# Optimization experiments

Hardware: AMD Instinct MI355X
Metric: run time of the kernel (lower is better)

## Reference

```python
import jax, jax.numpy as jnp
import numpy as np

BN_EPS = 1e-5

def setup_inputs() -> dict:
    key = jax.random.key(0)
    ks = jax.random.split(key, 4)
    B, C, H, W = 8, 64, 128, 128
    return {
        "x": jax.random.normal(ks[0], (B, C, H, W), jnp.float32),
        "w_reduce": jax.random.normal(ks[1], (C, C), jnp.float32) * 0.05,
        "b_reduce": jnp.zeros((C,), jnp.float32),
        "bn_gamma": jnp.ones((C,), jnp.float32),
        "bn_beta": jnp.zeros((C,), jnp.float32),
        "w_span": jax.random.normal(ks[2], (9, C), jnp.float32) * 0.05,
        "b_span": jnp.zeros((9,), jnp.float32),
        "w_conv2": jax.random.normal(ks[3], (C, C, 3, 3), jnp.float32) * 0.02,
        "b_conv2": jnp.zeros((C,), jnp.float32),
    }


def _involution(x, w_reduce, b_reduce, bn_gamma, bn_beta, w_span, b_span):
    # Involution2d: in_ch == out_ch so initial_mapping is Identity; groups=1, reduce_ratio=1, stride=1.
    B, C, H, W = x.shape
    # unfold 3x3, pad 1 -> patches [B, C, 9, H, W] (torch unfold ordering: C major, then kh, kw)
    xp = jnp.pad(x, ((0, 0), (0, 0), (1, 1), (1, 1)))
    patches = jnp.stack(
        [xp[:, :, i:i + H, j:j + W] for i in range(3) for j in range(3)], axis=2
    )  # [B, C, 9, H, W]
    # kernel generation: 1x1 conv -> BatchNorm2d (batch stats) -> ReLU -> 1x1 conv
    r = jnp.einsum('oc,bchw->bohw', w_reduce, x) + b_reduce[None, :, None, None]
    mu = r.mean(axis=(0, 2, 3), keepdims=True)
    var = r.var(axis=(0, 2, 3), keepdims=True)
    rn = (r - mu) * jax.lax.rsqrt(var + BN_EPS)
    rn = jax.nn.relu(rn * bn_gamma[None, :, None, None] + bn_beta[None, :, None, None])
    kern = jnp.einsum('kc,bchw->bkhw', w_span, rn) + b_span[None, :, None, None]  # [B, 9, H, W]
    # per-pixel dynamic kernel applied to patches, summed over kernel axis
    return jnp.einsum('bkhw,bckhw->bchw', kern, patches)


def reference(x, w_reduce, b_reduce, bn_gamma, bn_beta, w_span, b_span, w_conv2, b_conv2):
    z = jax.nn.softplus(_involution(x, w_reduce, b_reduce, bn_gamma, bn_beta, w_span, b_span))
    y = jax.lax.conv_general_dilated(z, w_conv2, window_strides=(1, 1), padding=((1, 1), (1, 1)))
    y = y + b_conv2[None, :, None, None]
    return jax.nn.softplus(y)
```

## Files before the change

kernel.cpp:

```cpp
#include <hip/hip_runtime.h>
#include <math.h>

#define H_ 128
#define W_ 128
#define C_ 64
#define B_ 8
#define HW 16384
#define NPIX (B_*HW)

typedef __attribute__((ext_vector_type(8))) short short8;
typedef __attribute__((ext_vector_type(4))) float f32x4;

__device__ __forceinline__ float softplus_fast(float v) {
    return fmaxf(v, 0.f) + __logf(1.f + __expf(-fabsf(v)));
}

__device__ __forceinline__ unsigned short f2bf(float f) {
    unsigned u = __builtin_bit_cast(unsigned, f);
    unsigned r = (u + 0x7fffu + ((u >> 16) & 1u)) >> 16;
    return (unsigned short)r;
}

__device__ __forceinline__ void gl_lds16(const float* g, float* l) {
    __builtin_amdgcn_global_load_lds(
        (const __attribute__((address_space(1))) void*)g,
        (__attribute__((address_space(3))) void*)l, 16, 0, 0);
}

__global__ __launch_bounds__(256) void k0_wtr(const float* __restrict__ w2,
                                              const float* __restrict__ wr,
                                              const float* __restrict__ wspan,
                                              unsigned short* __restrict__ wtr,
                                              unsigned short* __restrict__ wtr1,
                                              unsigned short* __restrict__ wtr2,
                                              float* __restrict__ stats)
{
    int t = blockIdx.x * 256 + threadIdx.x;
    if (t < 256) stats[t] = 0.f;
    if (t < 512) {
        int lane = t & 63, f = t >> 6;
        int mt = f >> 1, kh = f & 1;
        int o  = mt * 16 + (lane & 15);
        int c0 = kh * 32 + ((lane >> 4) << 3);
        uint4 pk;
        unsigned short* pv = (unsigned short*)&pk;
#pragma unroll
        for (int e = 0; e < 8; ++e)
            pv[e] = f2bf(wr[o * C_ + c0 + e]);
        *(uint4*)&wtr1[(size_t)t * 8] = pk;
    } else if (t < 640) {
        int tt = t - 512;
        int lane = tt & 63, kh = tt >> 6;
        int o  = lane & 15;
        int c0 = (kh << 5) + ((lane >> 4) << 3);
        uint4 pk;
        unsigned short* pv = (unsigned short*)&pk;
#pragma unroll
        for (int e = 0; e < 8; ++e)
            pv[e] = (o < 9) ? f2bf(wspan[o * C_ + c0 + e]) : (unsigned short)0;
        *(uint4*)&wtr2[(size_t)tt * 8] = pk;
    }
    if (t >= 4 * 18 * 64) return;
    int lane = t & 63;
    int f    = (t >> 6) % 18;
    int wv   = t / (18 * 64);
    int koff = f >> 1, ch = f & 1;
    int o = wv * 16 + (lane & 15);
    int cb = ch * 32 + ((lane >> 4) << 3);
    uint4 pk;
    unsigned short* pv = (unsigned short*)&pk;
#pragma unroll
    for (int e = 0; e < 8; ++e)
        pv[e] = f2bf(w2[(size_t)o * 576 + (size_t)(cb + e) * 9 + koff]);
    *(uint4*)&wtr[(size_t)t * 8] = pk;
}

__global__ __launch_bounds__(256) void k1_mfma(
    const float* __restrict__ x, const unsigned short* __restrict__ wtr1,
    const float* __restrict__ br, unsigned short* __restrict__ rb,
    float* __restrict__ stats)
{
    __shared__ unsigned short xb[256 * 64];
    __shared__ float brs[C_];
    __shared__ float ls[128];
    int tid = threadIdx.x;
    int blk = blockIdx.x;
    int pid0 = blk << 8;
    int b    = pid0 >> 14;
    int rem0 = pid0 & (HW - 1);
    const float* xbase = x + (((size_t)b * C_) << 14) + rem0;

    if (tid < C_) brs[tid] = br[tid];
    if (tid < 128) ls[tid] = 0.f;

    int p = tid;
#pragma unroll
    for (int m = 0; m < 8; ++m) {
        float tmp[8];
#pragma unroll
        for (int e = 0; e < 8; ++e)
            tmp[e] = xbase[((size_t)(m * 8 + e) << 14) + p];
        unsigned pk[4];
#pragma unroll
        for (int e = 0; e < 4; ++e)
            pk[e] = (unsigned)f2bf(tmp[2 * e]) | ((unsigned)f2bf(tmp[2 * e + 1]) << 16);
        *(uint4*)&xb[(p << 6) + ((m ^ (p & 7)) << 3)] = *(uint4*)pk;
    }

    int wid = tid >> 6, lane = tid & 63;
    int nl  = lane & 15;
    int kg  = lane >> 4;

    short8 af[8];
    const short8* wp = (const short8*)wtr1;
#pragma unroll
    for (int f = 0; f < 8; ++f) af[f] = wp[f * 64 + lane];

    f32x4 acc[4][4];
#pragma unroll
    for (int mt = 0; mt < 4; ++mt)
#pragma unroll
        for (int nt = 0; nt < 4; ++nt) acc[mt][nt] = (f32x4){0.f, 0.f, 0.f, 0.f};

    __syncthreads();

    int nbase = wid << 6;
#pragma unroll
    for (int nt = 0; nt < 4; ++nt) {
        int pp = nbase + (nt << 4) + nl;
#pragma unroll
        for (int kh = 0; kh < 2; ++kh) {
            int m = kh * 4 + kg;
            short8 bf = *(const short8*)&xb[(pp << 6) + ((m ^ (pp & 7)) << 3)];
#pragma unroll
            for (int mt = 0; mt < 4; ++mt)
                acc[mt][nt] = __builtin_amdgcn_mfma_f32_16x16x32_bf16(
                    af[mt * 2 + kh], bf, acc[mt][nt], 0, 0, 0);
        }
    }

    __syncthreads();

    float s_[16], q_[16];
#pragma unroll
    for (int i = 0; i < 16; ++i) { s_[i] = 0.f; q_[i] = 0.f; }

#pragma unroll
    for (int mt = 0; mt < 4; ++mt) {
        int c = (mt << 4) + (kg << 2);
        float b0 = brs[c], b1 = brs[c + 1], b2v = brs[c + 2], b3 = brs[c + 3];
        int chunk = c >> 3;
#pragma unroll
        for (int nt = 0; nt < 4; ++nt) {
            int pp = nbase + (nt << 4) + nl;
            f32x4 a = acc[mt][nt];
            float v0 = a[0] + b0, v1 = a[1] + b1, v2 = a[2] + b2v, v3 = a[3] + b3;
            s_[mt * 4 + 0] += v0; q_[mt * 4 + 0] += v0 * v0;
            s_[mt * 4 + 1] += v1; q_[mt * 4 + 1] += v1 * v1;
            s_[mt * 4 + 2] += v2; q_[mt * 4 + 2] += v2 * v2;
            s_[mt * 4 + 3] += v3; q_[mt * 4 + 3] += v3 * v3;
            unsigned lo = (unsigned)f2bf(v0) | ((unsigned)f2bf(v1) << 16);
            unsigned hi = (unsigned)f2bf(v2) | ((unsigned)f2bf(v3) << 16);
            unsigned* dst = (unsigned*)&xb[(pp << 6) + ((chunk ^ (pp & 7)) << 3) + ((kg & 1) << 2)];
            dst[0] = lo;
            dst[1] = hi;
        }
    }

#pragma unroll
    for (int i = 0; i < 16; ++i) {
#pragma unroll
        for (int m = 1; m <= 8; m <<= 1) {
            s_[i] += __shfl_xor(s_[i], m, 64);
            q_[i] += __shfl_xor(q_[i], m, 64);
        }
    }
    if (nl == 0) {
#pragma unroll
        for (int i = 0; i < 16; ++i) {
            int c = ((i >> 2) << 4) + (kg << 2) + (i & 3);
            atomicAdd(&ls[c], s_[i]);
            atomicAdd(&ls[64 + c], q_[i]);
        }
    }
    __syncthreads();
    if (tid < 128) atomicAdd(&stats[tid], ls[tid]);

    uint4* rp = (uint4*)(rb + ((size_t)(pid0 + p) << 6));
#pragma unroll
    for (int m = 0; m < 8; ++m)
        rp[m] = *(const uint4*)&xb[(p << 6) + ((m ^ (p & 7)) << 3)];
}

__global__ __launch_bounds__(256) void k3_involution(
    const float* __restrict__ x, const unsigned short* __restrict__ rb,
    const float* __restrict__ stats, const float* __restrict__ gamma,
    const float* __restrict__ beta, const unsigned short* __restrict__ wtr2,
    const float* __restrict__ bspan, unsigned short* __restrict__ zb)
{
    __shared__ float xh0[3456], xh1[3456];
    __shared__ unsigned zs[256 * 32];
    __shared__ float a_s[C_], c_s[C_];

    int tid = threadIdx.x;
    if (tid < C_) {
        float inv_n = 1.f / (float)NPIX;
        float mu  = stats[tid] * inv_n;
        float var = stats[C_ + tid] * inv_n - mu * mu;
        float is  = rsqrtf(var + 1e-5f);
        float a   = gamma[tid] * is;
        a_s[tid] = a;
        c_s[tid] = beta[tid] - mu * a;
    }

    int blk = blockIdx.x;
    int b = blk >> 6, t = blk & 63;
    int h0 = (t >> 3) << 4, w0 = (t & 7) << 4;
    int ty = tid >> 4, tx = tid & 15;
    int pix = ((h0 + ty) << 7) + (w0 + tx);
    int pid = (b << 14) + pix;
    const float* xb_ = x + (((size_t)b * C_) << 14);
    const float* zgz = stats + 128;

    int goff[4];
#pragma unroll
    for (int k = 0; k < 4; ++k) {
        int item = (k << 8) + tid;
        int c    = item / 108;
        int rem  = item - c * 108;
        int row  = rem / 6;
        int ii   = rem - row * 6;
        int gh   = h0 + row - 1;
        int gw0  = w0 - 4 + (ii << 2);
        bool ok = (item < 864) && ((unsigned)gh < 128u) && ((unsigned)gw0 < 128u);
        goff[k] = ok ? ((c << 14) + (gh << 7) + gw0) : -1;
    }

    auto stage = [&](int g, float* buf) {
#pragma unroll
        for (int k = 0; k < 4; ++k) {
            if (k < 3 || tid < 96) {
                int item = (k << 8) + tid;
                const float* src = (goff[k] >= 0) ? (xb_ + (g << 17) + goff[k]) : zgz;
                gl_lds16(src, buf + (item << 2));
            }
        }
    };

    int lane = tid & 63;
    int w_  = tid >> 6;
    int nl  = lane & 15;
    int kg  = lane >> 4;
    short8 af0 = ((const short8*)wtr2)[lane];
    short8 af1 = ((const short8*)wtr2)[64 + lane];

    stage(0, xh0);
    __syncthreads();
    stage(1, xh1);

    float aa[2][8], cc[2][8];
#pragma unroll
    for (int kh = 0; kh < 2; ++kh) {
        int cb = (kh << 5) + (kg << 3);
#pragma unroll
        for (int e = 0; e < 8; ++e) { aa[kh][e] = a_s[cb + e]; cc[kh][e] = c_s[cb + e]; }
    }

    f32x4 acc9[4];
#pragma unroll
    for (int nt = 0; nt < 4; ++nt) acc9[nt] = (f32x4){0.f, 0.f, 0.f, 0.f};

#pragma unroll
    for (int nt = 0; nt < 4; ++nt) {
        int prow = h0 + (w_ << 2) + nt;
        int pid2 = (b << 14) + (prow << 7) + w0 + nl;
#pragma unroll
        for (int kh = 0; kh < 2; ++kh) {
            uint4 rv = *(const uint4*)(rb + ((size_t)pid2 << 6) + (kh << 5) + (kg << 3));
            const unsigned* ru = (const unsigned*)&rv;
            unsigned po[4];
#pragma unroll
            for (int e2 = 0; e2 < 4; ++e2) {
                float lo = __builtin_bit_cast(float, ru[e2] << 16);
                float hi = __builtin_bit_cast(float, ru[e2] & 0xffff0000u);
                float r0 = fmaxf(aa[kh][2 * e2]     * lo + cc[kh][2 * e2],     0.f);
                float r1 = fmaxf(aa[kh][2 * e2 + 1] * hi + cc[kh][2 * e2 + 1], 0.f);
                po[e2] = (unsigned)f2bf(r0) | ((unsigned)f2bf(r1) << 16);
            }
            short8 bfrag = __builtin_bit_cast(short8, *(uint4*)po);
            acc9[nt] = __builtin_amdgcn_mfma_f32_16x16x32_bf16(
                kh ? af1 : af0, bfrag, acc9[nt], 0, 0, 0);
        }
    }

    float* kl = (float*)zs;
#pragma unroll
    for (int nt = 0; nt < 4; ++nt) {
        int px = (w_ << 6) + (nt << 4) + nl;
#pragma unroll
        for (int e = 0; e < 4; ++e) {
            int rr = (kg << 2) + e;
            if (rr < 9) kl[px * 9 + rr] = acc9[nt][e];
        }
    }
    __syncthreads();
    float kern[9];
#pragma unroll
    for (int k = 0; k < 9; ++k) kern[k] = kl[tid * 9 + k] + bspan[k];
    __syncthreads();

#pragma unroll 1
    for (int g = 0; g < 8; ++g) {
        if (g >= 1 && g < 7) stage(g + 1, (g & 1) ? xh0 : xh1);
        const float* xf = (g & 1) ? xh1 : xh0;
        unsigned pk[4];
#pragma unroll
        for (int cp = 0; cp < 4; ++cp) {
            const float* p0 = xf + (cp * 2) * 432 + ty * 24 + tx + 3;
            const float* p1 = p0 + 432;
            float acc0 = 0.f, acc1 = 0.f;
#pragma unroll
            for (int i = 0; i < 3; ++i)
#pragma unroll
                for (int j = 0; j < 3; ++j) {
                    float kv = kern[i * 3 + j];
                    acc0 += kv * p0[i * 24 + j];
                    acc1 += kv * p1[i * 24 + j];
                }
            pk[cp] = (unsigned)f2bf(softplus_fast(acc0))
                   | ((unsigned)f2bf(softplus_fast(acc1)) << 16);
        }
        *(uint4*)&zs[(tid << 5) + ((g ^ (tid & 7)) << 2)] = *(uint4*)pk;
        if (g < 7) __syncthreads();
    }

    uint4* zp = (uint4*)(zb + ((size_t)pid << 6));
#pragma unroll
    for (int k = 0; k < 8; ++k)
        zp[k] = *(const uint4*)&zs[(tid << 5) + ((k ^ (tid & 7)) << 2)];
}

__global__ __launch_bounds__(256) void k4_mfma(
    const unsigned short* __restrict__ zb, const unsigned short* __restrict__ wtr,
    const float* __restrict__ b2, float* __restrict__ out)
{
    __shared__ unsigned short zt[324 * 64];
    int tid = threadIdx.x;
    int blk = blockIdx.x;
    int b = blk >> 6;
    int t = blk & 63;
    int h0 = (t >> 3) << 4;
    int w0 = (t & 7) << 4;

    for (int idx = tid; idx < 324 * 8; idx += 256) {
        int p  = idx >> 3;
        int cg = idx & 7;
        int py = p / 18, px = p - py * 18;
        int gh = h0 + py - 1, gw = w0 + px - 1;
        uint4 v = make_uint4(0u, 0u, 0u, 0u);
        if ((unsigned)gh < 128u && (unsigned)gw < 128u)
            v = *(const uint4*)(zb + (((size_t)((b << 14) + (gh << 7) + gw)) << 6) + (cg << 3));
        *(uint4*)&zt[(p << 6) + ((cg ^ (p & 7)) << 3)] = v;
    }

    int wid  = tid >> 6, lane = tid & 63;
    int nl   = lane & 15;
    int kg   = lane >> 4;

    short8 wf[18];
    const short8* wp = (const short8*)wtr;
#pragma unroll
    for (int f = 0; f < 18; ++f)
        wf[f] = wp[(size_t)(wid * 18 + f) * 64 + lane];

    f32x4 acc[16];
#pragma unroll
    for (int nt = 0; nt < 16; ++nt) acc[nt] = (f32x4){0.f, 0.f, 0.f, 0.f};

    __syncthreads();

#pragma unroll
    for (int y = 0; y < 18; ++y) {
        short8 bf[6];
#pragma unroll
        for (int j = 0; j < 3; ++j)
#pragma unroll
            for (int ch = 0; ch < 2; ++ch) {
                int p  = y * 18 + j + nl;
                int cg = ch * 4 + kg;
                bf[j * 2 + ch] = *(const short8*)&zt[(p << 6) + ((cg ^ (p & 7)) << 3)];
            }
#pragma unroll
        for (int i = 0; i < 3; ++i) {
            int nt = y - i;
            if (nt >= 0 && nt < 16) {
#pragma unroll
                for (int j = 0; j < 3; ++j)
#pragma unroll
                    for (int ch = 0; ch < 2; ++ch)
                        acc[nt] = __builtin_amdgcn_mfma_f32_16x16x32_bf16(
                            wf[(i * 3 + j) * 2 + ch], bf[j * 2 + ch], acc[nt], 0, 0, 0);
            }
        }
    }

    float bias[4];
#pragma unroll
    for (int r = 0; r < 4; ++r) bias[r] = b2[(wid << 4) + (kg << 2) + r];

    size_t ob = ((size_t)b) << 20;
#pragma unroll
    for (int nt = 0; nt < 16; ++nt) {
        int h = h0 + nt;
#pragma unroll
        for (int r = 0; r < 4; ++r) {
            int o = (wid << 4) + (kg << 2) + r;
            float v = acc[nt][r] + bias[r];
            out[ob + ((size_t)o << 14) + (h << 7) + w0 + nl] = softplus_fast(v);
        }
    }
}

extern "C" void kernel_launch(void* const* d_in, const int* in_sizes, int n_in,
                              void* d_out, int out_size, void* d_ws, size_t ws_size,
                              hipStream_t stream)
{
    const float* x   = (const float*)d_in[0];
    const float* wr  = (const float*)d_in[1];
    const float* br  = (const float*)d_in[2];
    const float* gam = (const float*)d_in[3];
    const float* bet = (const float*)d_in[4];
    const float* wsp = (const float*)d_in[5];
    const float* bsp = (const float*)d_in[6];
    const float* w2  = (const float*)d_in[7];
    const float* b2  = (const float*)d_in[8];
    float* out = (float*)d_out;

    unsigned short* zb   = (unsigned short*)d_ws;
    unsigned short* wtr  = zb + (size_t)NPIX * C_;
    unsigned short* wtr1 = wtr + 4608 * 8;
    unsigned short* wtr2 = wtr1 + 512 * 8;
    float* stats = (float*)(wtr2 + 128 * 8);

    unsigned short* rb = (unsigned short*)d_out;

    k0_wtr<<<18, 256, 0, stream>>>(w2, wr, wsp, wtr, wtr1, wtr2, stats);
    k1_mfma<<<NPIX / 256, 256, 0, stream>>>(x, wtr1, br, rb, stats);
    k3_involution<<<NPIX / 256, 256, 0, stream>>>(x, rb, stats, gam, bet, wtr2, bsp, zb);
    k4_mfma<<<NPIX / 256, 256, 0, stream>>>(zb, wtr, b2, out);
}
```

Before: 80.84 us.

## Fuse involution and 3x3 conv kernels with halo recompute in shared memory

Merges the involution kernel and the MFMA 3x3 convolution into one kernel. Each block now computes the involution output for an 18x18 halo tile directly into shared memory, so the bf16 intermediate z no longer round-trips through global memory. The cost is recomputing the halo pixels (324 vs 256 per tile), larger x staging (20 rows), and more registers and shared memory per block, which may lower occupancy. The r buffer moves from the output buffer to the workspace.

```diff
diff --git a/kernel.cpp b/kernel.cpp
--- a/kernel.cpp
+++ b/kernel.cpp
@@ -192,14 +192,15 @@
         rp[m] = *(const uint4*)&xb[(p << 6) + ((m ^ (p & 7)) << 3)];
 }
 
-__global__ __launch_bounds__(256) void k3_involution(
+__global__ __launch_bounds__(256) void k34_fused(
     const float* __restrict__ x, const unsigned short* __restrict__ rb,
     const float* __restrict__ stats, const float* __restrict__ gamma,
     const float* __restrict__ beta, const unsigned short* __restrict__ wtr2,
-    const float* __restrict__ bspan, unsigned short* __restrict__ zb)
+    const float* __restrict__ bspan, const unsigned short* __restrict__ wtr,
+    const float* __restrict__ b2, float* __restrict__ out)
 {
-    __shared__ float xh0[3456], xh1[3456];
-    __shared__ unsigned zs[256 * 32];
+    __shared__ float xh0[8 * 20 * 24], xh1[8 * 20 * 24];
+    __shared__ unsigned short zt[324 * 64];
     __shared__ float a_s[C_], c_s[C_];
 
     int tid = threadIdx.x;
@@ -216,9 +217,6 @@
     int blk = blockIdx.x;
     int b = blk >> 6, t = blk & 63;
     int h0 = (t >> 3) << 4, w0 = (t & 7) << 4;
-    int ty = tid >> 4, tx = tid & 15;
-    int pix = ((h0 + ty) << 7) + (w0 + tx);
-    int pid = (b << 14) + pix;
     const float* xb_ = x + (((size_t)b * C_) << 14);
     const float* zgz = stats + 128;
 
@@ -226,20 +224,20 @@
 #pragma unroll
     for (int k = 0; k < 4; ++k) {
         int item = (k << 8) + tid;
-        int c    = item / 108;
-        int rem  = item - c * 108;
+        int c    = item / 120;
+        int rem  = item - c * 120;
         int row  = rem / 6;
         int ii   = rem - row * 6;
-        int gh   = h0 + row - 1;
-        int gw0  = w0 - 4 + (ii << 2);
-        bool ok = (item < 864) && ((unsigned)gh < 128u) && ((unsigned)gw0 < 128u);
-        goff[k] = ok ? ((c << 14) + (gh << 7) + gw0) : -1;
+        int gh   = h0 + row - 2;
+        int gw   = w0 - 4 + (ii << 2);
+        bool ok = (item < 960) && ((unsigned)gh < 128u) && ((unsigned)gw < 128u);
+        goff[k] = ok ? ((c << 14) + (gh << 7) + gw) : -1;
     }
 
     auto stage = [&](int g, float* buf) {
 #pragma unroll
         for (int k = 0; k < 4; ++k) {
-            if (k < 3 || tid < 96) {
+            if (k < 3 || tid < 192) {
                 int item = (k << 8) + tid;
                 const float* src = (goff[k] >= 0) ? (xb_ + (g << 17) + goff[k]) : zgz;
                 gl_lds16(src, buf + (item << 2));
@@ -266,118 +264,125 @@
         for (int e = 0; e < 8; ++e) { aa[kh][e] = a_s[cb + e]; cc[kh][e] = c_s[cb + e]; }
     }
 
-    f32x4 acc9[4];
-#pragma unroll
-    for (int nt = 0; nt < 4; ++nt) acc9[nt] = (f32x4){0.f, 0.f, 0.f, 0.f};
-
-#pragma unroll
-    for (int nt = 0; nt < 4; ++nt) {
-        int prow = h0 + (w_ << 2) + nt;
-        int pid2 = (b << 14) + (prow << 7) + w0 + nl;
-#pragma unroll
-        for (int kh = 0; kh < 2; ++kh) {
-            uint4 rv = *(const uint4*)(rb + ((size_t)pid2 << 6) + (kh << 5) + (kg << 3));
-            const unsigned* ru = (const unsigned*)&rv;
-            unsigned po[4];
-#pragma unroll
-            for (int e2 = 0; e2 < 4; ++e2) {
-                float lo = __builtin_bit_cast(float, ru[e2] << 16);
-                float hi = __builtin_bit_cast(float, ru[e2] & 0xffff0000u);
-                float r0 = fmaxf(aa[kh][2 * e2]     * lo + cc[kh][2 * e2],     0.f);
-                float r1 = fmaxf(aa[kh][2 * e2 + 1] * hi + cc[kh][2 * e2 + 1], 0.f);
-                po[e2] = (unsigned)f2bf(r0) | ((unsigned)f2bf(r1) << 16);
-            }
-            short8 bfrag = __builtin_bit_cast(short8, *(uint4*)po);
-            acc9[nt] = __builtin_amdgcn_mfma_f32_16x16x32_bf16(
-                kh ? af1 : af0, bfrag, acc9[nt], 0, 0, 0);
-        }
-    }
-
-    float* kl = (float*)zs;
-#pragma unroll
-    for (int nt = 0; nt < 4; ++nt) {
-        int px = (w_ << 6) + (nt << 4) + nl;
-#pragma unroll
-        for (int e = 0; e < 4; ++e) {
-            int rr = (kg << 2) + e;
-            if (rr < 9) kl[px * 9 + rr] = acc9[nt][e];
-        }
-    }
-    __syncthreads();
-    float kern[9];
-#pragma unroll
-    for (int k = 0; k < 9; ++k) kern[k] = kl[tid * 9 + k] + bspan[k];
-    __syncthreads();
+    float* kl = (float*)zt;
+#pragma unroll
+    for (int nt = 0; nt < 6; ++nt) {
+        int col = (nt << 2) + w_;
+        if (col < 21) {
+            int hp = (col << 4) + nl;
+            int py = hp / 18, px = hp - py * 18;
+            int gh = h0 + py - 1, gw = w0 + px - 1;
+            int ghc = min(max(gh, 0), 127), gwc = min(max(gw, 0), 127);
+            int pid2 = (b << 14) + (ghc << 7) + gwc;
+            f32x4 acc9 = (f32x4){0.f, 0.f, 0.f, 0.f};
+#pragma unroll
+            for (int kh = 0; kh < 2; ++kh) {
+                uint4 rv = *(const uint4*)(rb + ((size_t)pid2 << 6) + (kh << 5) + (kg << 3));
+                const unsigned* ru = (const unsigned*)&rv;
+                unsigned po[4];
+#pragma unroll
+                for (int e2 = 0; e2 < 4; ++e2) {
+                    float lo = __builtin_bit_cast(float, ru[e2] << 16);
+                    float hi = __builtin_bit_cast(float, ru[e2] & 0xffff0000u);
+                    float r0 = fmaxf(aa[kh][2 * e2]     * lo + cc[kh][2 * e2],     0.f);
+                    float r1 = fmaxf(aa[kh][2 * e2 + 1] * hi + cc[kh][2 * e2 + 1], 0.f);
+                    po[e2] = (unsigned)f2bf(r0) | ((unsigned)f2bf(r1) << 16);
+                }
+                short8 bfrag = __builtin_bit_cast(short8, *(uint4*)po);
+                acc9 = __builtin_amdgcn_mfma_f32_16x16x32_bf16(
+                    kh ? af1 : af0, bfrag, acc9, 0, 0, 0);
+            }
+#pragma unroll
+            for (int e = 0; e < 4; ++e) {
+                int rr = (kg << 2) + e;
+                if (rr < 9) kl[hp * 9 + rr] = acc9[e];
+            }
+        }
+    }
+    __syncthreads();
+
+    float kern0[9], kern1[9];
+#pragma unroll
+    for (int k = 0; k < 9; ++k) kern0[k] = kl[tid * 9 + k] + bspan[k];
+    bool has2 = tid < 68;
+    if (has2) {
+#pragma unroll
+        for (int k = 0; k < 9; ++k) kern1[k] = kl[(256 + tid) * 9 + k] + bspan[k];
+    }
+    __syncthreads();
+
+    int py0 = tid / 18, px0 = tid - py0 * 18;
+    bool ib0 = ((unsigned)(h0 + py0 - 1) < 128u) && ((unsigned)(w0 + px0 - 1) < 128u);
+    int hp1 = 256 + tid;
+    int py1 = hp1 / 18, px1 = hp1 - py1 * 18;
+    bool ib1 = has2 && ((unsigned)(h0 + py1 - 1) < 128u) && ((unsigned)(w0 + px1 - 1) < 128u);
+
+    short8 wf[18];
+    const short8* wp = (const short8*)wtr;
+#pragma unroll
+    for (int f = 0; f < 18; ++f)
+        wf[f] = wp[(size_t)(w_ * 18 + f) * 64 + lane];
 
 #pragma unroll 1
     for (int g = 0; g < 8; ++g) {
         if (g >= 1 && g < 7) stage(g + 1, (g & 1) ? xh0 : xh1);
         const float* xf = (g & 1) ? xh1 : xh0;
+
         unsigned pk[4];
-#pragma unroll
-        for (int cp = 0; cp < 4; ++cp) {
-            const float* p0 = xf + (cp * 2) * 432 + ty * 24 + tx + 3;
-            const float* p1 = p0 + 432;
-            float acc0 = 0.f, acc1 = 0.f;
-#pragma unroll
-            for (int i = 0; i < 3; ++i)
-#pragma unroll
-                for (int j = 0; j < 3; ++j) {
-                    float kv = kern[i * 3 + j];
-                    acc0 += kv * p0[i * 24 + j];
-                    acc1 += kv * p1[i * 24 + j];
+        if (ib0) {
+#pragma unroll
+            for (int cp = 0; cp < 4; ++cp) {
+                const float* p0 = xf + (cp * 2) * 480 + py0 * 24 + px0 + 2;
+                const float* p1 = p0 + 480;
+                float acc0 = 0.f, acc1 = 0.f;
+#pragma unroll
+                for (int i = 0; i < 3; ++i)
+#pragma unroll
+                    for (int j = 0; j < 3; ++j) {
+                        float kv = kern0[i * 3 + j];
+                        acc0 += kv * p0[i * 24 + j];
+                        acc1 += kv * p1[i * 24 + j];
+                    }
+                pk[cp] = (unsigned)f2bf(softplus_fast(acc0))
+                       | ((unsigned)f2bf(softplus_fast(acc1)) << 16);
+            }
+        } else {
+#pragma unroll
+            for (int cp = 0; cp < 4; ++cp) pk[cp] = 0u;
+        }
+        *(uint4*)&zt[(tid << 6) + ((g ^ (tid & 7)) << 3)] = *(uint4*)pk;
+
+        if (has2) {
+            if (ib1) {
+#pragma unroll
+                for (int cp = 0; cp < 4; ++cp) {
+                    const float* p0 = xf + (cp * 2) * 480 + py1 * 24 + px1 + 2;
+                    const float* p1 = p0 + 480;
+                    float acc0 = 0.f, acc1 = 0.f;
+#pragma unroll
+                    for (int i = 0; i < 3; ++i)
+#pragma unroll
+                        for (int j = 0; j < 3; ++j) {
+                            float kv = kern1[i * 3 + j];
+                            acc0 += kv * p0[i * 24 + j];
+                            acc1 += kv * p1[i * 24 + j];
+                        }
+                    pk[cp] = (unsigned)f2bf(softplus_fast(acc0))
+                           | ((unsigned)f2bf(softplus_fast(acc1)) << 16);
                 }
-            pk[cp] = (unsigned)f2bf(softplus_fast(acc0))
-                   | ((unsigned)f2bf(softplus_fast(acc1)) << 16);
-        }
-        *(uint4*)&zs[(tid << 5) + ((g ^ (tid & 7)) << 2)] = *(uint4*)pk;
+            } else {
+#pragma unroll
+                for (int cp = 0; cp < 4; ++cp) pk[cp] = 0u;
+            }
+            *(uint4*)&zt[(hp1 << 6) + ((g ^ (hp1 & 7)) << 3)] = *(uint4*)pk;
+        }
         if (g < 7) __syncthreads();
     }
-
-    uint4* zp = (uint4*)(zb + ((size_t)pid << 6));
-#pragma unroll
-    for (int k = 0; k < 8; ++k)
-        zp[k] = *(const uint4*)&zs[(tid << 5) + ((k ^ (tid & 7)) << 2)];
-}
-
-__global__ __launch_bounds__(256) void k4_mfma(
-    const unsigned short* __restrict__ zb, const unsigned short* __restrict__ wtr,
-    const float* __restrict__ b2, float* __restrict__ out)
-{
-    __shared__ unsigned short zt[324 * 64];
-    int tid = threadIdx.x;
-    int blk = blockIdx.x;
-    int b = blk >> 6;
-    int t = blk & 63;
-    int h0 = (t >> 3) << 4;
-    int w0 = (t & 7) << 4;
-
-    for (int idx = tid; idx < 324 * 8; idx += 256) {
-        int p  = idx >> 3;
-        int cg = idx & 7;
-        int py = p / 18, px = p - py * 18;
-        int gh = h0 + py - 1, gw = w0 + px - 1;
-        uint4 v = make_uint4(0u, 0u, 0u, 0u);
-        if ((unsigned)gh < 128u && (unsigned)gw < 128u)
-            v = *(const uint4*)(zb + (((size_t)((b << 14) + (gh << 7) + gw)) << 6) + (cg << 3));
-        *(uint4*)&zt[(p << 6) + ((cg ^ (p & 7)) << 3)] = v;
-    }
-
-    int wid  = tid >> 6, lane = tid & 63;
-    int nl   = lane & 15;
-    int kg   = lane >> 4;
-
-    short8 wf[18];
-    const short8* wp = (const short8*)wtr;
-#pragma unroll
-    for (int f = 0; f < 18; ++f)
-        wf[f] = wp[(size_t)(wid * 18 + f) * 64 + lane];
+    __syncthreads();
 
     f32x4 acc[16];
 #pragma unroll
     for (int nt = 0; nt < 16; ++nt) acc[nt] = (f32x4){0.f, 0.f, 0.f, 0.f};
-
-    __syncthreads();
 
 #pragma unroll
     for (int y = 0; y < 18; ++y) {
@@ -406,7 +411,7 @@
 
     float bias[4];
 #pragma unroll
-    for (int r = 0; r < 4; ++r) bias[r] = b2[(wid << 4) + (kg << 2) + r];
+    for (int r = 0; r < 4; ++r) bias[r] = b2[(w_ << 4) + (kg << 2) + r];
 
     size_t ob = ((size_t)b) << 20;
 #pragma unroll
@@ -414,7 +419,7 @@
         int h = h0 + nt;
 #pragma unroll
         for (int r = 0; r < 4; ++r) {
-            int o = (wid << 4) + (kg << 2) + r;
+            int o = (w_ << 4) + (kg << 2) + r;
             float v = acc[nt][r] + bias[r];
             out[ob + ((size_t)o << 14) + (h << 7) + w0 + nl] = softplus_fast(v);
         }
@@ -436,16 +441,14 @@
     const float* b2  = (const float*)d_in[8];
     float* out = (float*)d_out;
 
-    unsigned short* zb   = (unsigned short*)d_ws;
-    unsigned short* wtr  = zb + (size_t)NPIX * C_;
+    unsigned short* rb   = (unsigned short*)d_ws;
+    unsigned short* wtr  = rb + (size_t)NPIX * C_;
     unsigned short* wtr1 = wtr + 4608 * 8;
     unsigned short* wtr2 = wtr1 + 512 * 8;
     float* stats = (float*)(wtr2 + 128 * 8);
 
-    unsigned short* rb = (unsigned short*)d_out;
-
     k0_wtr<<<18, 256, 0, stream>>>(w2, wr, wsp, wtr, wtr1, wtr2, stats);
     k1_mfma<<<NPIX / 256, 256, 0, stream>>>(x, wtr1, br, rb, stats);
-    k3_involution<<<NPIX / 256, 256, 0, stream>>>(x, rb, stats, gam, bet, wtr2, bsp, zb);
-    k4_mfma<<<NPIX / 256, 256, 0, stream>>>(zb, wtr, b2, out);
-}
+    k34_fused<<<NPIX / 256, 256, 0, stream>>>(x, rb, stats, gam, bet, wtr2, bsp,
+                                              wtr, b2, out);
+}
```

After: 81.15 us. No clear change (+0.4%).
